# Optimization experiments

Measured on AMD Instinct MI355X. Metric: run time of the kernel, lower is better.

The kernel has to match this reference:

```python
import jax, jax.numpy as jnp
import numpy as np

HEADS = 16
DIM_HEAD = 64
BLOCK = 16
SEQ_LEN = 2048
NUM_BLOCKS = SEQ_LEN // BLOCK  # 128
NUM_RANDOM_BLOCKS = 32
LOCAL_WINDOW = 4
GLOBAL_BLOCKS = [0]


def make_layout():
    # Deterministic stand-in for DeepSpeed VariableSparsityConfig.make_layout
    # (local windows of 4 blocks + random blocks + global block columns/rows,
    #  then tril for unidirectional attention).
    rng = np.random.RandomState(0)
    nb = NUM_BLOCKS
    layout = np.zeros((nb, nb), dtype=bool)
    for w in range(0, nb, LOCAL_WINDOW):
        layout[w:w + LOCAL_WINDOW, w:w + LOCAL_WINDOW] = True
    rnd = rng.randint(0, nb, size=(nb, NUM_RANDOM_BLOCKS))
    layout[np.arange(nb)[:, None], rnd] = True
    for g in GLOBAL_BLOCKS:
        layout[:, g] = True
        layout[g, :] = True
    layout = np.tril(layout)  # unidirectional
    return jnp.asarray(layout)


def setup_inputs() -> dict:
    key = jax.random.key(0)
    k1, k2, k3 = jax.random.split(key, 3)
    dim = 1024
    inner = HEADS * DIM_HEAD  # 1024
    x = jax.random.normal(k1, (2, SEQ_LEN, dim), dtype=jnp.float32)
    w_qkv = jax.random.normal(k2, (dim, 3 * inner), dtype=jnp.float32) * 0.02
    w_out = jax.random.normal(k3, (inner, dim), dtype=jnp.float32) * 0.02
    b_out = jnp.zeros((dim,), dtype=jnp.float32)
    layout = make_layout()  # [128, 128] bool
    return {"x": x, "w_qkv": w_qkv, "w_out": w_out, "b_out": b_out, "layout": layout}


def reference(x, w_qkv, w_out, b_out, layout):
    b, n, _ = x.shape
    scale = DIM_HEAD ** -0.5
    qkv = x @ w_qkv  # [b, n, 3*h*d]
    q, k, v = jnp.split(qkv, 3, axis=-1)
    split_heads = lambda t: t.reshape(b, n, HEADS, DIM_HEAD).transpose(0, 2, 1, 3)
    q, k, v = split_heads(q), split_heads(k), split_heads(v)  # [b, h, n, d]

    scores = jnp.einsum('bhid,bhjd->bhij', q, k) * scale  # [b, h, n, n]
    neg = -jnp.finfo(scores.dtype).max
    # additive causal attn_mask (value = -finfo.max / 2, attn_mask_mode='add')
    causal = jnp.triu(jnp.ones((n, n), dtype=bool), 1)
    scores = scores + jnp.where(causal, neg / 2, jnp.zeros((), scores.dtype))
    # block-sparse layout: entries outside allowed blocks are fully masked
    allowed = jnp.repeat(jnp.repeat(layout, BLOCK, axis=0), BLOCK, axis=1)  # [n, n]
    scores = jnp.where(allowed, scores, neg)
    attn = jax.nn.softmax(scores, axis=-1)
    out = jnp.einsum('bhij,bhjd->bhid', attn, v)  # [b, h, n, d]
    out = out.transpose(0, 2, 1, 3).reshape(b, n, HEADS * DIM_HEAD)
    return out @ w_out + b_out
```

## Files before the change

### kernel.cpp

```cpp
#include <hip/hip_runtime.h>
#include <cstdint>
#include <cstddef>


typedef short bf8 __attribute__((ext_vector_type(8)));
typedef float f32x4 __attribute__((ext_vector_type(4)));
typedef unsigned short u16;
typedef unsigned int u32;

#define MFMA_BF16(a, b, c) __builtin_amdgcn_mfma_f32_16x16x32_bf16((a), (b), (c), 0, 0, 0)

constexpr int SEQ = 2048;
constexpr int NH = 16;
constexpr int DHD = 64;
constexpr int NBLK = 128;
constexpr int DIM = 1024;

__device__ __forceinline__ u16 f2bf(float f) {
  unsigned u = __float_as_uint(f);
  return (u16)((u + 0x7fffu + ((u >> 16) & 1u)) >> 16);
}
__device__ __forceinline__ u32 pack2bf(float a, float b) {
  return (u32)f2bf(a) | ((u32)f2bf(b) << 16);
}
__device__ __forceinline__ void gload_lds16(const u16* g, u16* l) {
  auto gp = (const __attribute__((address_space(1))) u16*)(g);
  auto lp = (__attribute__((address_space(3))) u16*)(l);
  __builtin_amdgcn_global_load_lds(gp, lp, 16, 0, 0);
}

__global__ __launch_bounds__(256) void convert_f32_bf16(
    const float* __restrict__ in, u16* __restrict__ out, int n) {
  int idx = (blockIdx.x * 256 + threadIdx.x) * 8;
  if (idx >= n) return;
  float4 a = *(const float4*)(in + idx);
  float4 b = *(const float4*)(in + idx + 4);
  *(ushort4*)(out + idx)     = make_ushort4(f2bf(a.x), f2bf(a.y), f2bf(a.z), f2bf(a.w));
  *(ushort4*)(out + idx + 4) = make_ushort4(f2bf(b.x), f2bf(b.y), f2bf(b.z), f2bf(b.w));
}

__global__ __launch_bounds__(256) void transpose_f32_bf16(
    const float* __restrict__ in, u16* __restrict__ out, int R, int C) {
  __shared__ u16 tile[64][72];
  int c0 = blockIdx.x * 64, r0 = blockIdx.y * 64;
  int t = threadIdx.x;
  int rr = t >> 4, cc = (t & 15) * 4;
  #pragma unroll
  for (int p = 0; p < 64; p += 16) {
    float4 v = *(const float4*)(in + (size_t)(r0 + rr + p) * C + c0 + cc);
    tile[rr + p][cc + 0] = f2bf(v.x);
    tile[rr + p][cc + 1] = f2bf(v.y);
    tile[rr + p][cc + 2] = f2bf(v.z);
    tile[rr + p][cc + 3] = f2bf(v.w);
  }
  __syncthreads();
  int oc = t >> 3, orr = (t & 7) * 8;
  #pragma unroll
  for (int p = 0; p < 64; p += 32) {
    u16 tmp[8];
    #pragma unroll
    for (int qy = 0; qy < 8; qy++) tmp[qy] = tile[orr + qy][oc + p];
    u16* dst = out + (size_t)(c0 + oc + p) * R + r0 + orr;
    *(ushort4*)(dst)     = make_ushort4(tmp[0], tmp[1], tmp[2], tmp[3]);
    *(ushort4*)(dst + 4) = make_ushort4(tmp[4], tmp[5], tmp[6], tmp[7]);
  }
}

__global__ __launch_bounds__(64) void build_lists(
    const unsigned char* __restrict__ lay, int* __restrict__ cnt, int* __restrict__ cols) {
  int i = blockIdx.x;
  int lane = threadIdx.x;
  const uint4* l4 = (const uint4*)lay;
  u32 acc = 0;
  #pragma unroll
  for (int it = 0; it < 16; it++) {
    uint4 v = l4[it * 64 + lane];
    acc |= ((v.x | v.y | v.z | v.w) & 0xFFFFFF00u);
  }
  bool as_int32 = (__ballot(acc != 0) == 0ULL);
  const int* li = (const int*)lay;
  int j0 = lane, j1 = lane + 64;
  bool p0 = (j0 <= i) && (as_int32 ? (li[i * 128 + j0] != 0) : (lay[i * 128 + j0] != 0));
  bool p1 = (j1 <= i) && (as_int32 ? (li[i * 128 + j1] != 0) : (lay[i * 128 + j1] != 0));
  unsigned long long m0 = __ballot(p0), m1 = __ballot(p1);
  unsigned long long lt = (1ULL << lane) - 1ULL;
  int base0 = __popcll(m0);
  if (p0) cols[i * 128 + __popcll(m0 & lt)] = j0;
  if (p1) cols[i * 128 + base0 + __popcll(m1 & lt)] = j1;
  if (lane == 0) cnt[i] = base0 + __popcll(m1);
}

constexpr int BM = 128, BN = 128, BK = 32;

__global__ __launch_bounds__(256) void gemm_bt(
    const u16* __restrict__ A, const u16* __restrict__ Bt,
    int M, int N, int K, int mode,
    u16* __restrict__ oq, u16* __restrict__ okk, u16* __restrict__ ov,
    float* __restrict__ of, const float* __restrict__ bias) {
  __shared__ u16 sA[BM * BK];
  __shared__ u16 sB[BN * BK];
  __shared__ u16 ebuf[32 * 132];
  int tid = threadIdx.x;
  int lane = tid & 63, wave = tid >> 6;
  int quad = lane >> 4, l16 = lane & 15;
  int wr = wave >> 1, wc = wave & 1;
  int bm0 = blockIdx.y * BM, bn0 = blockIdx.x * BN;

  f32x4 acc[4][4];
  #pragma unroll
  for (int i = 0; i < 4; i++)
    #pragma unroll
    for (int j = 0; j < 4; j++) acc[i][j] = (f32x4){0.f, 0.f, 0.f, 0.f};

  int srow = wave * 32 + (lane >> 2);
  int schunk = (lane & 3) * 8;
  for (int k0 = 0; k0 < K; k0 += BK) {
    const u16* ga = A  + (size_t)(bm0 + srow) * K + k0 + schunk;
    const u16* gb = Bt + (size_t)(bn0 + srow) * K + k0 + schunk;
    gload_lds16(ga,          sA + (wave * 32) * BK);
    gload_lds16(ga + 16 * K, sA + (wave * 32 + 16) * BK);
    gload_lds16(gb,          sB + (wave * 32) * BK);
    gload_lds16(gb + 16 * K, sB + (wave * 32 + 16) * BK);
    __syncthreads();
    bf8 af[4], bfr[4];
    #pragma unroll
    for (int i = 0; i < 4; i++)
      af[i] = *(const bf8*)(sA + (wr * 64 + i * 16 + l16) * BK + quad * 8);
    #pragma unroll
    for (int j = 0; j < 4; j++)
      bfr[j] = *(const bf8*)(sB + (wc * 64 + j * 16 + l16) * BK + quad * 8);
    #pragma unroll
    for (int i = 0; i < 4; i++)
      #pragma unroll
      for (int j = 0; j < 4; j++)
        acc[i][j] = MFMA_BF16(af[i], bfr[j], acc[i][j]);
    __syncthreads();
  }

  if (mode == 0) {
    int which = bn0 >> 10;
    if (which == 2) {
      #pragma unroll
      for (int j = 0; j < 4; j++) {
        int c = bn0 + wc * 64 + j * 16 + l16;
        int h = (c & 1023) >> 6, dd = c & 63;
        #pragma unroll
        for (int i = 0; i < 4; i++) {
          int r0 = bm0 + wr * 64 + i * 16;
          int b = r0 >> 11, nn0 = r0 & 2047, jb = nn0 >> 4;
          u16* dst = ov + ((size_t)((b * NH + h) * NBLK + jb) * DHD + dd) * 16 + quad * 4;
          *(ushort4*)dst = make_ushort4(f2bf(acc[i][j][0]), f2bf(acc[i][j][1]),
                                        f2bf(acc[i][j][2]), f2bf(acc[i][j][3]));
        }
      }
    } else {
      u16* dstbase = (which == 0) ? oq : okk;
      #pragma unroll
      for (int j = 0; j < 4; j++) {
        __syncthreads();
        #pragma unroll
        for (int i = 0; i < 4; i++) {
          int row = wr * 64 + i * 16 + quad * 4;
          *(uint2*)&ebuf[(wc * 16 + l16) * 132 + row] =
              make_uint2(pack2bf(acc[i][j][0], acc[i][j][1]),
                         pack2bf(acc[i][j][2], acc[i][j][3]));
        }
        __syncthreads();
        int row = tid >> 1, wcr = tid & 1;
        union { u16 t[16]; uint4 q[2]; } tv;
        #pragma unroll
        for (int dd = 0; dd < 16; dd++) tv.t[dd] = ebuf[(wcr * 16 + dd) * 132 + row];
        int h = ((bn0 + wcr * 64 + j * 16) & 1023) >> 6;
        int r = bm0 + row;
        int b = r >> 11, nn = r & 2047;
        u16* dst = dstbase + ((size_t)(b * NH + h) * SEQ + nn) * DHD + j * 16;
        *(uint4*)(dst) = tv.q[0];
        *(uint4*)(dst + 8) = tv.q[1];
      }
    }
  } else {
    #pragma unroll
    for (int j = 0; j < 4; j++) {
      int c = bn0 + wc * 64 + j * 16 + l16;
      float bv = bias[c];
      #pragma unroll
      for (int i = 0; i < 4; i++) {
        int rbase = bm0 + wr * 64 + i * 16 + quad * 4;
        #pragma unroll
        for (int ii = 0; ii < 4; ii++)
          of[(size_t)(rbase + ii) * N + c] = acc[i][j][ii] + bv;
      }
    }
  }
}

__global__ __launch_bounds__(256) void attn_sparse(
    const u16* __restrict__ q, const u16* __restrict__ k, const u16* __restrict__ vblk,
    const int* __restrict__ cnt, const int* __restrict__ cols,
    u16* __restrict__ aout) {
  __shared__ u32 pbuf[4][320];
  __shared__ float obuf[2][64 * 20];
  __shared__ float lbuf[2][64];
  int wave = threadIdx.x >> 6, lane = threadIdx.x & 63;
  int quad = lane >> 4, l16 = lane & 15;
  int qslot = wave >> 1, half = wave & 1;
  int blk = blockIdx.x;
  int bh = blk >> 6;
  int qb = (blk & 63) * 2 + qslot;
  const float scale = 0.125f;
  u32* pbw = pbuf[wave];

  const u16* qp = q + ((size_t)bh * SEQ + qb * 16) * DHD + l16 * DHD + quad * 8;
  bf8 qa0 = *(const bf8*)(qp);
  bf8 qa1 = *(const bf8*)(qp + 32);

  float l_i = 0.f;
  f32x4 o[4];
  #pragma unroll
  for (int t = 0; t < 4; t++) o[t] = (f32x4){0.f, 0.f, 0.f, 0.f};

  int count = cnt[qb];
  const int* mc = cols + qb * NBLK;

  bf8 bufA[8], bufB[8];
  int ja0 = 0, ja1 = 0, jb0b = 0, jb1b = 0;
  bool hvA = false, hvB = false;

  auto ldpair = [&](int p, bf8* kv, int& o0, int& o1, bool& ohv) {
    o0 = mc[p];
    ohv = (p + 1 < count);
    o1 = ohv ? mc[p + 1] : o0;
    const u16* kp0 = k + ((size_t)bh * SEQ + o0 * 16) * DHD + l16 * DHD + quad * 8;
    kv[0] = *(const bf8*)(kp0); kv[1] = *(const bf8*)(kp0 + 32);
    const u16* kp1 = k + ((size_t)bh * SEQ + o1 * 16) * DHD + l16 * DHD + quad * 8;
    kv[2] = *(const bf8*)(kp1); kv[3] = *(const bf8*)(kp1 + 32);
    int jq = (quad < 2) ? o0 : o1;
    const u16* vp = vblk + (size_t)(bh * NBLK + jq) * 1024 + l16 * 16 + (quad & 1) * 8;
    kv[4] = *(const bf8*)(vp);
    kv[5] = *(const bf8*)(vp + 256);
    kv[6] = *(const bf8*)(vp + 512);
    kv[7] = *(const bf8*)(vp + 768);
  };

  int myp = half * 2;
  if (myp < count) ldpair(myp, bufA, ja0, ja1, hvA);
  if (myp + 4 < count) ldpair(myp + 4, bufB, jb0b, jb1b, hvB);

  for (int p = myp; p < count; p += 4) {
    f32x4 S0 = (f32x4){0.f, 0.f, 0.f, 0.f};
    S0 = MFMA_BF16(bufA[0], qa0, S0);
    S0 = MFMA_BF16(bufA[1], qa1, S0);
    f32x4 S1 = (f32x4){0.f, 0.f, 0.f, 0.f};
    S1 = MFMA_BF16(bufA[2], qa0, S1);
    S1 = MFMA_BF16(bufA[3], qa1, S1);

    float e0[4], e1[4];
    #pragma unroll
    for (int r = 0; r < 4; r++) {
      int kl = quad * 4 + r;
      float s0 = S0[r] * scale;
      if (ja0 == qb && kl > l16) s0 = -1e38f;
      float s1 = hvA ? S1[r] * scale : -1e38f;
      if (hvA && ja1 == qb && kl > l16) s1 = -1e38f;
      e0[r] = __expf(s0);
      e1[r] = __expf(s1);
      l_i += e0[r] + e1[r];
    }

    *(uint2*)(&pbw[l16 * 20 + quad * 2]) =
        make_uint2(pack2bf(e0[0], e0[1]), pack2bf(e0[2], e0[3]));
    *(uint2*)(&pbw[l16 * 20 + 8 + quad * 2]) =
        make_uint2(pack2bf(e1[0], e1[1]), pack2bf(e1[2], e1[3]));
    union { uint4 w; bf8 v; } pf;
    pf.w = *(const uint4*)(&pbw[l16 * 20 + quad * 4]);

    o[0] = MFMA_BF16(bufA[4], pf.v, o[0]);
    o[1] = MFMA_BF16(bufA[5], pf.v, o[1]);
    o[2] = MFMA_BF16(bufA[6], pf.v, o[2]);
    o[3] = MFMA_BF16(bufA[7], pf.v, o[3]);

    #pragma unroll
    for (int z = 0; z < 8; z++) bufA[z] = bufB[z];
    ja0 = jb0b; ja1 = jb1b; hvA = hvB;
    if (p + 8 < count) ldpair(p + 8, bufB, jb0b, jb1b, hvB);
  }

  if (half == 1) {
    #pragma unroll
    for (int t = 0; t < 4; t++)
      *(f32x4*)(&obuf[qslot][lane * 20 + t * 4]) = o[t];
    lbuf[qslot][lane] = l_i;
  }
  __syncthreads();
  if (half == 0) {
    #pragma unroll
    for (int t = 0; t < 4; t++)
      o[t] += *(const f32x4*)(&obuf[qslot][lane * 20 + t * 4]);
    float l = l_i + lbuf[qslot][lane];
    l += __shfl_xor(l, 16);
    l += __shfl_xor(l, 32);
    float inv = 1.0f / l;
    int b = bh >> 4, h = bh & 15;
    int n = qb * 16 + l16;
    u16* dst = aout + ((size_t)b * SEQ + n) * DIM + h * DHD;
    #pragma unroll
    for (int t = 0; t < 4; t++) {
      ushort4 st = make_ushort4(f2bf(o[t][0] * inv), f2bf(o[t][1] * inv),
                                f2bf(o[t][2] * inv), f2bf(o[t][3] * inv));
      *(ushort4*)(dst + t * 16 + quad * 4) = st;
    }
  }
}

extern "C" void kernel_launch(void* const* d_in, const int* in_sizes, int n_in,
                              void* d_out, int out_size, void* d_ws, size_t ws_size,
                              hipStream_t stream) {
  const float* x      = (const float*)d_in[0];
  const float* w_qkv  = (const float*)d_in[1];
  const float* w_out  = (const float*)d_in[2];
  const float* b_out  = (const float*)d_in[3];
  const unsigned char* layout = (const unsigned char*)d_in[4];
  float* out = (float*)d_out;

  char* ws = (char*)d_ws;
  u16* xbf   = (u16*)(ws);
  u16* wqkvT = (u16*)(ws + (8u  << 20));
  u16* woutT = (u16*)(ws + (14u << 20) + (512u << 10));
  u16* qB    = (u16*)(ws + (17u << 20));
  u16* kB    = (u16*)(ws + (25u << 20));
  u16* vblk  = (u16*)(ws + (33u << 20));
  u16* aout  = (u16*)(ws + (41u << 20));
  int* cnt   = (int*)(ws + (49u << 20));
  int* cols  = (int*)(ws + (49u << 20) + 4096);

  convert_f32_bf16<<<2048, 256, 0, stream>>>(x, xbf, 4096 * 1024);
  transpose_f32_bf16<<<dim3(48, 16, 1), 256, 0, stream>>>(w_qkv, wqkvT, 1024, 3072);
  transpose_f32_bf16<<<dim3(16, 16, 1), 256, 0, stream>>>(w_out, woutT, 1024, 1024);
  build_lists<<<128, 64, 0, stream>>>(layout, cnt, cols);
  gemm_bt<<<dim3(24, 32, 1), 256, 0, stream>>>(xbf, wqkvT, 4096, 3072, 1024, 0,
                                               qB, kB, vblk, nullptr, nullptr);
  attn_sparse<<<2048, 256, 0, stream>>>(qB, kB, vblk, cnt, cols, aout);
  gemm_bt<<<dim3(8, 32, 1), 256, 0, stream>>>(aout, woutT, 4096, 1024, 1024, 1,
                                              nullptr, nullptr, nullptr, out, b_out);
}
```

Measured before the change: 201.3 us.

## Fuse prep kernels into one launch and retile GEMMs with BK=64

Merges the f32→bf16 conversion, both weight transposes and layout list building into a single prep kernel dispatched by block index, which cuts three launches. Splits the generic GEMM into specialised QKV and output kernels and doubles the K tile to 64, halving the number of barriers per K loop. The output GEMM narrows its N tile to 64 to launch more blocks. The QKV epilogue now reuses the staging shared memory and does one transpose pass instead of four synchronised ones, at the cost of larger LDS use per block.

After: 200.2 us. No clear change (-0.5%).

```diff
diff --git a/kernel.cpp b/kernel.cpp
--- a/kernel.cpp
+++ b/kernel.cpp
@@ -29,47 +29,56 @@
   __builtin_amdgcn_global_load_lds(gp, lp, 16, 0, 0);
 }
 
-__global__ __launch_bounds__(256) void convert_f32_bf16(
-    const float* __restrict__ in, u16* __restrict__ out, int n) {
-  int idx = (blockIdx.x * 256 + threadIdx.x) * 8;
-  if (idx >= n) return;
-  float4 a = *(const float4*)(in + idx);
-  float4 b = *(const float4*)(in + idx + 4);
-  *(ushort4*)(out + idx)     = make_ushort4(f2bf(a.x), f2bf(a.y), f2bf(a.z), f2bf(a.w));
-  *(ushort4*)(out + idx + 4) = make_ushort4(f2bf(b.x), f2bf(b.y), f2bf(b.z), f2bf(b.w));
-}
-
-__global__ __launch_bounds__(256) void transpose_f32_bf16(
-    const float* __restrict__ in, u16* __restrict__ out, int R, int C) {
+__global__ __launch_bounds__(256) void prep(
+    const float* __restrict__ x, u16* __restrict__ xbf,
+    const float* __restrict__ wqkv, u16* __restrict__ wqkvT,
+    const float* __restrict__ wout, u16* __restrict__ woutT,
+    const unsigned char* __restrict__ lay,
+    int* __restrict__ cnt, int* __restrict__ cols) {
   __shared__ u16 tile[64][72];
-  int c0 = blockIdx.x * 64, r0 = blockIdx.y * 64;
+  int bid = blockIdx.x;
   int t = threadIdx.x;
-  int rr = t >> 4, cc = (t & 15) * 4;
-  #pragma unroll
-  for (int p = 0; p < 64; p += 16) {
-    float4 v = *(const float4*)(in + (size_t)(r0 + rr + p) * C + c0 + cc);
-    tile[rr + p][cc + 0] = f2bf(v.x);
-    tile[rr + p][cc + 1] = f2bf(v.y);
-    tile[rr + p][cc + 2] = f2bf(v.z);
-    tile[rr + p][cc + 3] = f2bf(v.w);
-  }
-  __syncthreads();
-  int oc = t >> 3, orr = (t & 7) * 8;
-  #pragma unroll
-  for (int p = 0; p < 64; p += 32) {
-    u16 tmp[8];
-    #pragma unroll
-    for (int qy = 0; qy < 8; qy++) tmp[qy] = tile[orr + qy][oc + p];
-    u16* dst = out + (size_t)(c0 + oc + p) * R + r0 + orr;
-    *(ushort4*)(dst)     = make_ushort4(tmp[0], tmp[1], tmp[2], tmp[3]);
-    *(ushort4*)(dst + 4) = make_ushort4(tmp[4], tmp[5], tmp[6], tmp[7]);
-  }
-}
-
-__global__ __launch_bounds__(64) void build_lists(
-    const unsigned char* __restrict__ lay, int* __restrict__ cnt, int* __restrict__ cols) {
-  int i = blockIdx.x;
-  int lane = threadIdx.x;
+
+  if (bid < 2048) {
+    int idx = (bid * 256 + t) * 8;
+    float4 a = *(const float4*)(x + idx);
+    float4 b = *(const float4*)(x + idx + 4);
+    *(ushort4*)(xbf + idx)     = make_ushort4(f2bf(a.x), f2bf(a.y), f2bf(a.z), f2bf(a.w));
+    *(ushort4*)(xbf + idx + 4) = make_ushort4(f2bf(b.x), f2bf(b.y), f2bf(b.z), f2bf(b.w));
+    return;
+  }
+  bid -= 2048;
+  if (bid < 768 + 256) {
+    const float* in; u16* out; int C, bx, by;
+    if (bid < 768) { in = wqkv; out = wqkvT; C = 3072; bx = bid % 48; by = bid / 48; }
+    else { int r = bid - 768; in = wout; out = woutT; C = 1024; bx = r % 16; by = r / 16; }
+    const int R = 1024;
+    int c0 = bx * 64, r0 = by * 64;
+    int rr = t >> 4, cc = (t & 15) * 4;
+    #pragma unroll
+    for (int p = 0; p < 64; p += 16) {
+      float4 v = *(const float4*)(in + (size_t)(r0 + rr + p) * C + c0 + cc);
+      tile[rr + p][cc + 0] = f2bf(v.x);
+      tile[rr + p][cc + 1] = f2bf(v.y);
+      tile[rr + p][cc + 2] = f2bf(v.z);
+      tile[rr + p][cc + 3] = f2bf(v.w);
+    }
+    __syncthreads();
+    int oc = t >> 3, orr = (t & 7) * 8;
+    #pragma unroll
+    for (int p = 0; p < 64; p += 32) {
+      u16 tmp[8];
+      #pragma unroll
+      for (int qy = 0; qy < 8; qy++) tmp[qy] = tile[orr + qy][oc + p];
+      u16* dst = out + (size_t)(c0 + oc + p) * R + r0 + orr;
+      *(ushort4*)(dst)     = make_ushort4(tmp[0], tmp[1], tmp[2], tmp[3]);
+      *(ushort4*)(dst + 4) = make_ushort4(tmp[4], tmp[5], tmp[6], tmp[7]);
+    }
+    return;
+  }
+  bid -= 1024;
+  int wave = t >> 6, lane = t & 63;
+  int i = bid * 4 + wave;
   const uint4* l4 = (const uint4*)lay;
   u32 acc = 0;
   #pragma unroll
@@ -90,21 +99,17 @@
   if (lane == 0) cnt[i] = base0 + __popcll(m1);
 }
 
-constexpr int BM = 128, BN = 128, BK = 32;
-
-__global__ __launch_bounds__(256) void gemm_bt(
+__global__ __launch_bounds__(256) void gemm_qkv(
     const u16* __restrict__ A, const u16* __restrict__ Bt,
-    int M, int N, int K, int mode,
-    u16* __restrict__ oq, u16* __restrict__ okk, u16* __restrict__ ov,
-    float* __restrict__ of, const float* __restrict__ bias) {
-  __shared__ u16 sA[BM * BK];
-  __shared__ u16 sB[BN * BK];
-  __shared__ u16 ebuf[32 * 132];
-  int tid = threadIdx.x;
-  int lane = tid & 63, wave = tid >> 6;
+    u16* __restrict__ oq, u16* __restrict__ okk, u16* __restrict__ ov) {
+  __shared__ u16 smem[16896];
+  u16* sA = smem;
+  u16* sB = smem + 8192;
+  const int K = 1024;
+  int tid = threadIdx.x, lane = tid & 63, wave = tid >> 6;
   int quad = lane >> 4, l16 = lane & 15;
   int wr = wave >> 1, wc = wave & 1;
-  int bm0 = blockIdx.y * BM, bn0 = blockIdx.x * BN;
+  int bm0 = blockIdx.y * 128, bn0 = blockIdx.x * 128;
 
   f32x4 acc[4][4];
   #pragma unroll
@@ -112,84 +117,148 @@
     #pragma unroll
     for (int j = 0; j < 4; j++) acc[i][j] = (f32x4){0.f, 0.f, 0.f, 0.f};
 
-  int srow = wave * 32 + (lane >> 2);
-  int schunk = (lane & 3) * 8;
-  for (int k0 = 0; k0 < K; k0 += BK) {
-    const u16* ga = A  + (size_t)(bm0 + srow) * K + k0 + schunk;
-    const u16* gb = Bt + (size_t)(bn0 + srow) * K + k0 + schunk;
-    gload_lds16(ga,          sA + (wave * 32) * BK);
-    gload_lds16(ga + 16 * K, sA + (wave * 32 + 16) * BK);
-    gload_lds16(gb,          sB + (wave * 32) * BK);
-    gload_lds16(gb + 16 * K, sB + (wave * 32 + 16) * BK);
-    __syncthreads();
-    bf8 af[4], bfr[4];
-    #pragma unroll
-    for (int i = 0; i < 4; i++)
-      af[i] = *(const bf8*)(sA + (wr * 64 + i * 16 + l16) * BK + quad * 8);
-    #pragma unroll
-    for (int j = 0; j < 4; j++)
-      bfr[j] = *(const bf8*)(sB + (wc * 64 + j * 16 + l16) * BK + quad * 8);
-    #pragma unroll
-    for (int i = 0; i < 4; i++)
+  int srow8 = lane >> 3;
+  int schunk = (lane & 7) * 8;
+  for (int k0 = 0; k0 < K; k0 += 64) {
+    #pragma unroll
+    for (int r = 0; r < 4; r++) {
+      int row = wave * 8 + r * 32 + srow8;
+      gload_lds16(A + (size_t)(bm0 + row) * K + k0 + schunk,
+                  sA + (wave * 8 + r * 32) * 64);
+    }
+    #pragma unroll
+    for (int r = 0; r < 4; r++) {
+      int row = wave * 8 + r * 32 + srow8;
+      gload_lds16(Bt + (size_t)(bn0 + row) * K + k0 + schunk,
+                  sB + (wave * 8 + r * 32) * 64);
+    }
+    __syncthreads();
+    #pragma unroll
+    for (int ks = 0; ks < 2; ks++) {
+      bf8 af[4], bfr[4];
+      #pragma unroll
+      for (int i = 0; i < 4; i++)
+        af[i] = *(const bf8*)(sA + (wr * 64 + i * 16 + l16) * 64 + ks * 32 + quad * 8);
       #pragma unroll
       for (int j = 0; j < 4; j++)
-        acc[i][j] = MFMA_BF16(af[i], bfr[j], acc[i][j]);
-    __syncthreads();
-  }
-
-  if (mode == 0) {
-    int which = bn0 >> 10;
-    if (which == 2) {
-      #pragma unroll
-      for (int j = 0; j < 4; j++) {
-        int c = bn0 + wc * 64 + j * 16 + l16;
-        int h = (c & 1023) >> 6, dd = c & 63;
+        bfr[j] = *(const bf8*)(sB + (wc * 64 + j * 16 + l16) * 64 + ks * 32 + quad * 8);
+      #pragma unroll
+      for (int i = 0; i < 4; i++)
         #pragma unroll
-        for (int i = 0; i < 4; i++) {
-          int r0 = bm0 + wr * 64 + i * 16;
-          int b = r0 >> 11, nn0 = r0 & 2047, jb = nn0 >> 4;
-          u16* dst = ov + ((size_t)((b * NH + h) * NBLK + jb) * DHD + dd) * 16 + quad * 4;
-          *(ushort4*)dst = make_ushort4(f2bf(acc[i][j][0]), f2bf(acc[i][j][1]),
-                                        f2bf(acc[i][j][2]), f2bf(acc[i][j][3]));
-        }
-      }
-    } else {
-      u16* dstbase = (which == 0) ? oq : okk;
-      #pragma unroll
-      for (int j = 0; j < 4; j++) {
-        __syncthreads();
-        #pragma unroll
-        for (int i = 0; i < 4; i++) {
-          int row = wr * 64 + i * 16 + quad * 4;
-          *(uint2*)&ebuf[(wc * 16 + l16) * 132 + row] =
-              make_uint2(pack2bf(acc[i][j][0], acc[i][j][1]),
-                         pack2bf(acc[i][j][2], acc[i][j][3]));
-        }
-        __syncthreads();
-        int row = tid >> 1, wcr = tid & 1;
-        union { u16 t[16]; uint4 q[2]; } tv;
-        #pragma unroll
-        for (int dd = 0; dd < 16; dd++) tv.t[dd] = ebuf[(wcr * 16 + dd) * 132 + row];
-        int h = ((bn0 + wcr * 64 + j * 16) & 1023) >> 6;
-        int r = bm0 + row;
-        int b = r >> 11, nn = r & 2047;
-        u16* dst = dstbase + ((size_t)(b * NH + h) * SEQ + nn) * DHD + j * 16;
-        *(uint4*)(dst) = tv.q[0];
-        *(uint4*)(dst + 8) = tv.q[1];
-      }
-    }
-  } else {
+        for (int j = 0; j < 4; j++)
+          acc[i][j] = MFMA_BF16(af[i], bfr[j], acc[i][j]);
+    }
+    __syncthreads();
+  }
+
+  int which = bn0 >> 10;
+  if (which == 2) {
     #pragma unroll
     for (int j = 0; j < 4; j++) {
       int c = bn0 + wc * 64 + j * 16 + l16;
-      float bv = bias[c];
+      int h = (c & 1023) >> 6, dd = c & 63;
       #pragma unroll
       for (int i = 0; i < 4; i++) {
-        int rbase = bm0 + wr * 64 + i * 16 + quad * 4;
+        int r0 = bm0 + wr * 64 + i * 16;
+        int b = r0 >> 11, nn0 = r0 & 2047, jb = nn0 >> 4;
+        u16* dst = ov + ((size_t)((b * NH + h) * NBLK + jb) * DHD + dd) * 16 + quad * 4;
+        *(ushort4*)dst = make_ushort4(f2bf(acc[i][j][0]), f2bf(acc[i][j][1]),
+                                      f2bf(acc[i][j][2]), f2bf(acc[i][j][3]));
+      }
+    }
+  } else {
+    u16* dstbase = (which == 0) ? oq : okk;
+    #pragma unroll
+    for (int j = 0; j < 4; j++) {
+      int col = wc * 64 + j * 16 + l16;
+      #pragma unroll
+      for (int i = 0; i < 4; i++) {
+        int row = wr * 64 + i * 16 + quad * 4;
+        *(uint2*)&smem[col * 132 + row] =
+            make_uint2(pack2bf(acc[i][j][0], acc[i][j][1]),
+                       pack2bf(acc[i][j][2], acc[i][j][3]));
+      }
+    }
+    __syncthreads();
+    int r = tid >> 1, half = tid & 1;
+    int rglob = bm0 + r;
+    int b = rglob >> 11, nn = rglob & 2047;
+    int h = ((bn0 & 1023) >> 6) + half;
+    #pragma unroll
+    for (int j = 0; j < 4; j++) {
+      union { u16 t[16]; uint4 q[2]; } tv;
+      #pragma unroll
+      for (int dd = 0; dd < 16; dd++)
+        tv.t[dd] = smem[(half * 64 + j * 16 + dd) * 132 + r];
+      u16* dst = dstbase + ((size_t)(b * NH + h) * SEQ + nn) * DHD + j * 16;
+      *(uint4*)(dst) = tv.q[0];
+      *(uint4*)(dst + 8) = tv.q[1];
+    }
+  }
+}
+
+__global__ __launch_bounds__(256) void gemm_out(
+    const u16* __restrict__ A, const u16* __restrict__ Bt,
+    float* __restrict__ of, const float* __restrict__ bias) {
+  __shared__ u16 smem[12288];
+  u16* sA = smem;
+  u16* sB = smem + 8192;
+  const int K = 1024, N = 1024;
+  int tid = threadIdx.x, lane = tid & 63, wave = tid >> 6;
+  int quad = lane >> 4, l16 = lane & 15;
+  int wr = wave >> 1, wc = wave & 1;
+  int bm0 = blockIdx.y * 128, bn0 = blockIdx.x * 64;
+
+  f32x4 acc[4][2];
+  #pragma unroll
+  for (int i = 0; i < 4; i++)
+    #pragma unroll
+    for (int j = 0; j < 2; j++) acc[i][j] = (f32x4){0.f, 0.f, 0.f, 0.f};
+
+  int srow8 = lane >> 3;
+  int schunk = (lane & 7) * 8;
+  for (int k0 = 0; k0 < K; k0 += 64) {
+    #pragma unroll
+    for (int r = 0; r < 4; r++) {
+      int row = wave * 8 + r * 32 + srow8;
+      gload_lds16(A + (size_t)(bm0 + row) * K + k0 + schunk,
+                  sA + (wave * 8 + r * 32) * 64);
+    }
+    #pragma unroll
+    for (int r = 0; r < 2; r++) {
+      int row = wave * 8 + r * 32 + srow8;
+      gload_lds16(Bt + (size_t)(bn0 + row) * K + k0 + schunk,
+                  sB + (wave * 8 + r * 32) * 64);
+    }
+    __syncthreads();
+    #pragma unroll
+    for (int ks = 0; ks < 2; ks++) {
+      bf8 af[4], bfr[2];
+      #pragma unroll
+      for (int i = 0; i < 4; i++)
+        af[i] = *(const bf8*)(sA + (wr * 64 + i * 16 + l16) * 64 + ks * 32 + quad * 8);
+      #pragma unroll
+      for (int j = 0; j < 2; j++)
+        bfr[j] = *(const bf8*)(sB + (wc * 32 + j * 16 + l16) * 64 + ks * 32 + quad * 8);
+      #pragma unroll
+      for (int i = 0; i < 4; i++)
         #pragma unroll
-        for (int ii = 0; ii < 4; ii++)
-          of[(size_t)(rbase + ii) * N + c] = acc[i][j][ii] + bv;
-      }
+        for (int j = 0; j < 2; j++)
+          acc[i][j] = MFMA_BF16(af[i], bfr[j], acc[i][j]);
+    }
+    __syncthreads();
+  }
+
+  #pragma unroll
+  for (int j = 0; j < 2; j++) {
+    int c = bn0 + wc * 32 + j * 16 + l16;
+    float bv = bias[c];
+    #pragma unroll
+    for (int i = 0; i < 4; i++) {
+      int rbase = bm0 + wr * 64 + i * 16 + quad * 4;
+      #pragma unroll
+      for (int ii = 0; ii < 4; ii++)
+        of[(size_t)(rbase + ii) * N + c] = acc[i][j][ii] + bv;
     }
   }
 }
@@ -333,13 +402,9 @@
   int* cnt   = (int*)(ws + (49u << 20));
   int* cols  = (int*)(ws + (49u << 20) + 4096);
 
-  convert_f32_bf16<<<2048, 256, 0, stream>>>(x, xbf, 4096 * 1024);
-  transpose_f32_bf16<<<dim3(48, 16, 1), 256, 0, stream>>>(w_qkv, wqkvT, 1024, 3072);
-  transpose_f32_bf16<<<dim3(16, 16, 1), 256, 0, stream>>>(w_out, woutT, 1024, 1024);
-  build_lists<<<128, 64, 0, stream>>>(layout, cnt, cols);
-  gemm_bt<<<dim3(24, 32, 1), 256, 0, stream>>>(xbf, wqkvT, 4096, 3072, 1024, 0,
-                                               qB, kB, vblk, nullptr, nullptr);
+  prep<<<3104, 256, 0, stream>>>(x, xbf, w_qkv, wqkvT, w_out, woutT,
+                                 layout, cnt, cols);
+  gemm_qkv<<<dim3(24, 32, 1), 256, 0, stream>>>(xbf, wqkvT, qB, kB, vblk);
   attn_sparse<<<2048, 256, 0, stream>>>(qB, kB, vblk, cnt, cols, aout);
-  gemm_bt<<<dim3(8, 32, 1), 256, 0, stream>>>(aout, woutT, 4096, 1024, 1024, 1,
-                                              nullptr, nullptr, nullptr, out, b_out);
-}
+  gemm_out<<<dim3(16, 32, 1), 256, 0, stream>>>(aout, woutT, out, b_out);
+}
```
